# Optimization experiments

Hardware: AMD Instinct MI355X
Metric: run time of the kernel (lower is better)

The kernel has to match this reference:

```python
import jax, jax.numpy as jnp
import numpy as np

NUM_LATENTS = 8192
LATENT_DIM = 256


def setup_inputs() -> dict:
    key = jax.random.key(0)
    kx, kw = jax.random.split(key)
    x = jax.random.normal(kx, (32, 512, LATENT_DIM), dtype=jnp.float32)
    # codebook init: uniform(-1/K, 1/K), matching nn.Embedding init in the module
    bound = 1.0 / NUM_LATENTS
    codebook = jax.random.uniform(
        kw, (NUM_LATENTS, LATENT_DIM), dtype=jnp.float32, minval=-bound, maxval=bound
    )
    return {"x": x, "codebook": codebook}


def reference(x, codebook):
    # torch.cdist(x, W) followed by argmin. Since sqrt is monotone, argmin over
    # squared Euclidean distance gives identical indices; we expand
    x2 = jnp.sum(x * x, axis=-1, keepdims=True)              # [B, T, 1]
    w2 = jnp.sum(codebook * codebook, axis=-1)               # [K]
    xw = jnp.einsum("btd,kd->btk", x, codebook)              # [B, T, K]
    dist2 = x2 - 2.0 * xw + w2                               # [B, T, K]
    indices = jnp.argmin(dist2, axis=-1)                     # [B, T] int
    z = codebook[indices]                                    # [B, T, D]
    # straight-through estimator: z_q = x + stop_grad(z - x)
    z_q = x + jax.lax.stop_gradient(z - x)
    return (z_q, z, x, indices)
```

## Files before the change

### kernel.cpp

```cpp
#include <hip/hip_runtime.h>
#include <hip/hip_bf16.h>
#include <cstddef>
#include <cstdint>

#define M_TOK   16384
#define N_CODE  8192
#define K_DIM   256
#define NSPLIT  4
#define BM      128
#define BN      256
#define BK      32
#define KSTEPS  (K_DIM / BK)
#define TILES   ((N_CODE / NSPLIT) / BN)
#define TOTAL_STEPS (TILES * KSTEPS)
#define STEP_BYTES 49152
#define XH_OFF 0
#define XL_OFF 8192
#define WH_OFF 16384
#define WL_OFF 32768

typedef short bf16x8 __attribute__((ext_vector_type(8)));
typedef float f32x4  __attribute__((ext_vector_type(4)));

__device__ __forceinline__ unsigned short f2bf_rne(float f) {
    unsigned u = __float_as_uint(f);
    unsigned r = u + 0x7FFFu + ((u >> 16) & 1u);
    return (unsigned short)(r >> 16);
}
__device__ __forceinline__ float bf2f(unsigned short h) {
    union { unsigned u; float f; } c; c.u = ((unsigned)h) << 16; return c.f;
}

__device__ __forceinline__ void gload16(const void* g, void* l) {
    __builtin_amdgcn_global_load_lds(
        (const __attribute__((address_space(1))) void*)g,
        (__attribute__((address_space(3))) void*)l, 16, 0, 0);
}

__global__ void vq_prep(const float* __restrict__ x, const float* __restrict__ cb,
                        unsigned short* __restrict__ xh, unsigned short* __restrict__ xl,
                        unsigned short* __restrict__ wh, unsigned short* __restrict__ wl,
                        float* __restrict__ x2, float* __restrict__ w2) {
    int gt   = blockIdx.x * blockDim.x + threadIdx.x;
    int row  = gt >> 6;
    int lane = gt & 63;
    if (row >= M_TOK + N_CODE) return;
    const float* src; unsigned short *dh, *dl; float* dn;
    if (row < M_TOK) {
        src = x + (size_t)row * K_DIM;
        dh = xh + (size_t)row * K_DIM; dl = xl + (size_t)row * K_DIM; dn = x2 + row;
    } else {
        int r = row - M_TOK;
        src = cb + (size_t)r * K_DIM;
        dh = wh + (size_t)r * K_DIM; dl = wl + (size_t)r * K_DIM; dn = w2 + r;
    }
    float4 v = ((const float4*)src)[lane];
    unsigned short h0 = f2bf_rne(v.x), h1 = f2bf_rne(v.y);
    unsigned short h2 = f2bf_rne(v.z), h3 = f2bf_rne(v.w);
    unsigned short l0 = f2bf_rne(v.x - bf2f(h0)), l1 = f2bf_rne(v.y - bf2f(h1));
    unsigned short l2 = f2bf_rne(v.z - bf2f(h2)), l3 = f2bf_rne(v.w - bf2f(h3));
    ushort4 hv; hv.x = h0; hv.y = h1; hv.z = h2; hv.w = h3;
    ushort4 lv; lv.x = l0; lv.y = l1; lv.z = l2; lv.w = l3;
    ((ushort4*)dh)[lane] = hv;
    ((ushort4*)dl)[lane] = lv;
    float s = v.x*v.x + v.y*v.y + v.z*v.z + v.w*v.w;
    #pragma unroll
    for (int off = 32; off > 0; off >>= 1) s += __shfl_down(s, off);
    if (lane == 0) *dn = s;
}

__global__ __launch_bounds__(512, 2)
void vq_main_mfma(const unsigned short* __restrict__ xh, const unsigned short* __restrict__ xl,
                  const unsigned short* __restrict__ wh, const unsigned short* __restrict__ wl,
                  const float* __restrict__ x2, const float* __restrict__ w2,
                  float* __restrict__ pminv, int* __restrict__ pmini) {
    __shared__ __align__(1024) char sb[3][STEP_BYTES];
    __shared__ float red_d[BM][4];
    __shared__ int   red_i[BM][4];

    const int fid   = blockIdx.y * NSPLIT + blockIdx.x;
    const int xcd   = fid & 7;
    const int split = xcd & 3;
    const int mtile = ((xcd >> 2) << 6) + (fid >> 3);
    const int gm    = mtile * BM;

    const int tid   = threadIdx.x;
    const int w     = tid >> 6;
    const int lane  = tid & 63;
    const int wr    = w >> 2;
    const int wc    = w & 3;
    const int quad  = lane >> 4;
    const int l15   = lane & 15;

    const int srow4 = lane >> 2;
    const int sg    = (lane & 3) ^ ((lane >> 3) & 3);

    const char* xhp = (const char*)xh;
    const char* xlp = (const char*)xl;
    const char* whp = (const char*)wh;
    const char* wlp = (const char*)wl;

    const size_t xg0 = (size_t)(gm + w*16 + srow4) * (K_DIM*2) + (size_t)sg*16;
    const size_t wg0 = (size_t)(w*32 + srow4) * (K_DIM*2) + (size_t)sg*16;
    const size_t wg1 = wg0 + (size_t)16 * (K_DIM*2);
    const unsigned lx = (unsigned)w*1024 + (unsigned)lane*16;
    const unsigned lw = (unsigned)w*2048 + (unsigned)lane*16;

    float x2r[16];
    #pragma unroll
    for (int rt = 0; rt < 4; ++rt)
        #pragma unroll
        for (int reg = 0; reg < 4; ++reg)
            x2r[rt*4+reg] = x2[gm + wr*64 + rt*16 + quad*4 + reg];

    float minv[16];
    int   mini[16];
    #pragma unroll
    for (int i = 0; i < 16; ++i) { minv[i] = 3.4e38f; mini[i] = 0; }

    auto stage = [&](int s, char* buf) {
        const size_t kb  = (size_t)(s & (KSTEPS-1)) * (BK*2);
        const size_t nbo = ((size_t)(split*(N_CODE/NSPLIT) + (s >> 3) * BN)) * (K_DIM*2);
        gload16(xhp + xg0 + kb,        buf + XH_OFF + lx);
        gload16(xlp + xg0 + kb,        buf + XL_OFF + lx);
        gload16(whp + nbo + wg0 + kb,  buf + WH_OFF + lw);
        gload16(whp + nbo + wg1 + kb,  buf + WH_OFF + lw + 1024);
        gload16(wlp + nbo + wg0 + kb,  buf + WL_OFF + lw);
        gload16(wlp + nbo + wg1 + kb,  buf + WL_OFF + lw + 1024);
    };

    char* bufA = &sb[0][0];
    char* bufB = &sb[1][0];
    char* bufC = &sb[2][0];
    stage(0, bufA); stage(1, bufB); stage(2, bufC);

    const int slb = (quad ^ ((l15 >> 1) & 3)) * 16;

    for (int tile = 0; tile < TILES; ++tile) {
        f32x4 acc[4][4];
        #pragma unroll
        for (int rt = 0; rt < 4; ++rt)
            #pragma unroll
            for (int ct = 0; ct < 4; ++ct)
                acc[rt][ct] = (f32x4){0.f, 0.f, 0.f, 0.f};

        for (int kcs = 0; kcs < KSTEPS; ++kcs) {
            const int step = tile * KSTEPS + kcs;

            if (step < TOTAL_STEPS - 2)       asm volatile("s_waitcnt vmcnt(12)" ::: "memory");
            else if (step == TOTAL_STEPS - 2) asm volatile("s_waitcnt vmcnt(6)" ::: "memory");
            else                              asm volatile("s_waitcnt vmcnt(0)" ::: "memory");
            __builtin_amdgcn_s_barrier();
            __builtin_amdgcn_sched_barrier(0);

            bf16x8 ah[4], al[4], bh[4], bl[4];
            #pragma unroll
            for (int rt = 0; rt < 4; ++rt) {
                const int off = (wr*64 + rt*16 + l15) * (BK*2) + slb;
                ah[rt] = *(const bf16x8*)(bufA + XH_OFF + off);
                al[rt] = *(const bf16x8*)(bufA + XL_OFF + off);
            }
            #pragma unroll
            for (int ct = 0; ct < 4; ++ct) {
                const int off = (wc*64 + ct*16 + l15) * (BK*2) + slb;
                bh[ct] = *(const bf16x8*)(bufA + WH_OFF + off);
                bl[ct] = *(const bf16x8*)(bufA + WL_OFF + off);
            }
            asm volatile("s_waitcnt lgkmcnt(0)" ::: "memory");
            __builtin_amdgcn_sched_barrier(0);
            __builtin_amdgcn_s_barrier();
            __builtin_amdgcn_sched_barrier(0);

            const int sn = step + 3;
            if (sn < TOTAL_STEPS) stage(sn, bufA);

            __builtin_amdgcn_s_setprio(1);
            #pragma unroll
            for (int rt = 0; rt < 4; ++rt)
                #pragma unroll
                for (int ct = 0; ct < 4; ++ct) {
                    acc[rt][ct] = __builtin_amdgcn_mfma_f32_16x16x32_bf16(al[rt], bh[ct], acc[rt][ct], 0, 0, 0);
                    acc[rt][ct] = __builtin_amdgcn_mfma_f32_16x16x32_bf16(ah[rt], bl[ct], acc[rt][ct], 0, 0, 0);
                    acc[rt][ct] = __builtin_amdgcn_mfma_f32_16x16x32_bf16(ah[rt], bh[ct], acc[rt][ct], 0, 0, 0);
                }
            __builtin_amdgcn_s_setprio(0);

            char* t = bufA; bufA = bufB; bufB = bufC; bufC = t;
        }

        const int nb = split * (N_CODE / NSPLIT) + tile * BN;
        float w2c[4];
        int   cidx[4];
        #pragma unroll
        for (int ct = 0; ct < 4; ++ct) {
            cidx[ct] = nb + wc*64 + ct*16 + l15;
            w2c[ct]  = w2[cidx[ct]];
        }
        #pragma unroll
        for (int rt = 0; rt < 4; ++rt)
            #pragma unroll
            for (int ct = 0; ct < 4; ++ct) {
                #pragma unroll
                for (int reg = 0; reg < 4; ++reg) {
                    float d = (x2r[rt*4+reg] - 2.0f * acc[rt][ct][reg]) + w2c[ct];
                    int r16 = rt*4 + reg;
                    if (d < minv[r16]) { minv[r16] = d; mini[r16] = cidx[ct]; }
                }
            }
    }

    #pragma unroll
    for (int r16 = 0; r16 < 16; ++r16) {
        float d  = minv[r16];
        int   ix = mini[r16];
        #pragma unroll
        for (int off = 1; off < 16; off <<= 1) {
            float od = __shfl_xor(d, off);
            int   oi = __shfl_xor(ix, off);
            if (od < d || (od == d && oi < ix)) { d = od; ix = oi; }
        }
        if (l15 == 0) {
            int row_local = wr*64 + (r16 >> 2)*16 + quad*4 + (r16 & 3);
            red_d[row_local][wc] = d;
            red_i[row_local][wc] = ix;
        }
    }
    __syncthreads();
    if (tid < BM) {
        float d  = red_d[tid][0];
        int   ix = red_i[tid][0];
        #pragma unroll
        for (int j = 1; j < 4; ++j) {
            float dj = red_d[tid][j];
            int   ij = red_i[tid][j];
            if (dj < d || (dj == d && ij < ix)) { d = dj; ix = ij; }
        }
        pminv[(size_t)(gm + tid) * NSPLIT + split] = d;
        pmini[(size_t)(gm + tid) * NSPLIT + split] = ix;
    }
}

__global__ void vq_gather(const float* __restrict__ x, const float* __restrict__ cb,
                          const float* __restrict__ pminv, const int* __restrict__ pmini,
                          float* __restrict__ out) {
    int t = blockIdx.x * blockDim.x + threadIdx.x;
    int m = t >> 6;
    int q = t & 63;

    float d  = pminv[(size_t)m * NSPLIT + (q & (NSPLIT-1))];
    int   ix = pmini[(size_t)m * NSPLIT + (q & (NSPLIT-1))];
    #pragma unroll
    for (int off = 1; off < NSPLIT; off <<= 1) {
        float od = __shfl_xor(d, off);
        int   oi = __shfl_xor(ix, off);
        if (od < d || (od == d && oi < ix)) { d = od; ix = oi; }
    }

    float4 xv = ((const float4*)x)[t];
    float4 zv = ((const float4*)cb)[(size_t)ix * 64 + q];
    float4 zq;
    zq.x = xv.x + (zv.x - xv.x);
    zq.y = xv.y + (zv.y - xv.y);
    zq.z = xv.z + (zv.z - xv.z);
    zq.w = xv.w + (zv.w - xv.w);
    float4* o = (float4*)out;
    const int ELEM4 = M_TOK * 64;
    o[t]           = zq;
    o[t + ELEM4]   = zv;
    o[t + 2*ELEM4] = xv;
    if (q == 0) out[(size_t)3 * M_TOK * K_DIM + m] = (float)ix;
}

extern "C" void kernel_launch(void* const* d_in, const int* in_sizes, int n_in,
                              void* d_out, int out_size, void* d_ws, size_t ws_size,
                              hipStream_t stream) {
    const float* x  = (const float*)d_in[0];
    const float* cb = (const float*)d_in[1];
    float* out = (float*)d_out;

    char* p = (char*)d_ws;
    unsigned short* xh = (unsigned short*)p;  p += (size_t)M_TOK  * K_DIM * 2;
    unsigned short* xl = (unsigned short*)p;  p += (size_t)M_TOK  * K_DIM * 2;
    unsigned short* wh = (unsigned short*)p;  p += (size_t)N_CODE * K_DIM * 2;
    unsigned short* wl = (unsigned short*)p;  p += (size_t)N_CODE * K_DIM * 2;
    float* x2    = (float*)p;  p += (size_t)M_TOK * 4;
    float* w2    = (float*)p;  p += (size_t)N_CODE * 4;
    float* pminv = (float*)p;  p += (size_t)M_TOK * NSPLIT * 4;
    int*   pmini = (int*)p;    p += (size_t)M_TOK * NSPLIT * 4;

    {
        int waves = M_TOK + N_CODE;
        vq_prep<<<(waves * 64 + 255) / 256, 256, 0, stream>>>(x, cb, xh, xl, wh, wl, x2, w2);
    }
    {
        dim3 grid(NSPLIT, M_TOK / BM);
        vq_main_mfma<<<grid, 512, 0, stream>>>(xh, xl, wh, wl, x2, w2, pminv, pmini);
    }
    {
        int t = M_TOK * (K_DIM / 4);
        vq_gather<<<t / 256, 256, 0, stream>>>(x, cb, pminv, pmini, out);
    }
}
```

Baseline: 295.7 us.

## Register double-buffer LDS fragments and stage norms in shared memory

The main loop now loads the next k-step's A/B fragments from LDS into a second register set while MFMAs run on the current set. This drops one barrier per step and hides LDS read latency behind compute. The MFMAs are regrouped into three passes (lo*hi, hi*lo, hi*hi). The x2 and w2 norms are prefetched into shared memory with async global-to-LDS loads instead of being kept in registers or read from global per tile. In exchange it uses twice as many fragment registers, which risks spills at the 512x2 launch bounds, and the vmcnt accounting changes with the extra loads.

```diff
diff --git a/kernel.cpp b/kernel.cpp
--- a/kernel.cpp
+++ b/kernel.cpp
@@ -75,6 +75,8 @@
                   const float* __restrict__ x2, const float* __restrict__ w2,
                   float* __restrict__ pminv, int* __restrict__ pmini) {
     __shared__ __align__(1024) char sb[3][STEP_BYTES];
+    __shared__ float x2s[BM];
+    __shared__ float w2s[N_CODE/NSPLIT];
     __shared__ float red_d[BM][4];
     __shared__ int   red_i[BM][4];
 
@@ -103,111 +105,146 @@
     const size_t xg0 = (size_t)(gm + w*16 + srow4) * (K_DIM*2) + (size_t)sg*16;
     const size_t wg0 = (size_t)(w*32 + srow4) * (K_DIM*2) + (size_t)sg*16;
     const size_t wg1 = wg0 + (size_t)16 * (K_DIM*2);
-    const unsigned lx = (unsigned)w*1024 + (unsigned)lane*16;
-    const unsigned lw = (unsigned)w*2048 + (unsigned)lane*16;
-
-    float x2r[16];
-    #pragma unroll
-    for (int rt = 0; rt < 4; ++rt)
-        #pragma unroll
-        for (int reg = 0; reg < 4; ++reg)
-            x2r[rt*4+reg] = x2[gm + wr*64 + rt*16 + quad*4 + reg];
-
-    float minv[16];
-    int   mini[16];
-    #pragma unroll
-    for (int i = 0; i < 16; ++i) { minv[i] = 3.4e38f; mini[i] = 0; }
+    const unsigned lxu = (unsigned)w*1024;
+    const unsigned lwu = (unsigned)w*2048;
 
     auto stage = [&](int s, char* buf) {
         const size_t kb  = (size_t)(s & (KSTEPS-1)) * (BK*2);
         const size_t nbo = ((size_t)(split*(N_CODE/NSPLIT) + (s >> 3) * BN)) * (K_DIM*2);
-        gload16(xhp + xg0 + kb,        buf + XH_OFF + lx);
-        gload16(xlp + xg0 + kb,        buf + XL_OFF + lx);
-        gload16(whp + nbo + wg0 + kb,  buf + WH_OFF + lw);
-        gload16(whp + nbo + wg1 + kb,  buf + WH_OFF + lw + 1024);
-        gload16(wlp + nbo + wg0 + kb,  buf + WL_OFF + lw);
-        gload16(wlp + nbo + wg1 + kb,  buf + WL_OFF + lw + 1024);
+        gload16(xhp + xg0 + kb,        buf + XH_OFF + lxu);
+        gload16(xlp + xg0 + kb,        buf + XL_OFF + lxu);
+        gload16(whp + nbo + wg0 + kb,  buf + WH_OFF + lwu);
+        gload16(whp + nbo + wg1 + kb,  buf + WH_OFF + lwu + 1024);
+        gload16(wlp + nbo + wg0 + kb,  buf + WL_OFF + lwu);
+        gload16(wlp + nbo + wg1 + kb,  buf + WL_OFF + lwu + 1024);
     };
 
-    char* bufA = &sb[0][0];
-    char* bufB = &sb[1][0];
-    char* bufC = &sb[2][0];
-    stage(0, bufA); stage(1, bufB); stage(2, bufC);
+    gload16((const char*)w2 + (size_t)split*(N_CODE/NSPLIT)*4 + (size_t)w*1024 + (size_t)lane*16,
+            (char*)w2s + lxu);
+    if (w == 0 && lane < 32)
+        gload16((const char*)x2 + (size_t)gm*4 + (size_t)lane*16, (char*)x2s);
+    char* cur = &sb[0][0];
+    char* nxt = &sb[1][0];
+    char* bfar = &sb[2][0];
+    stage(0, cur); stage(1, nxt); stage(2, bfar);
+    asm volatile("s_waitcnt vmcnt(12)" ::: "memory");
+    __builtin_amdgcn_s_barrier();
+    __builtin_amdgcn_sched_barrier(0);
 
     const int slb = (quad ^ ((l15 >> 1) & 3)) * 16;
 
+    bf16x8 ah0[4], al0[4], bh0[4], bl0[4];
+    bf16x8 ah1[4], al1[4], bh1[4], bl1[4];
+
+    #pragma unroll
+    for (int rt = 0; rt < 4; ++rt) {
+        const int off = (wr*64 + rt*16 + l15)*(BK*2) + slb;
+        ah0[rt] = *(const bf16x8*)(cur + XH_OFF + off);
+        al0[rt] = *(const bf16x8*)(cur + XL_OFF + off);
+    }
+    #pragma unroll
+    for (int ct = 0; ct < 4; ++ct) {
+        const int off = (wc*64 + ct*16 + l15)*(BK*2) + slb;
+        bh0[ct] = *(const bf16x8*)(cur + WH_OFF + off);
+        bl0[ct] = *(const bf16x8*)(cur + WL_OFF + off);
+    }
+    asm volatile("s_waitcnt lgkmcnt(0)" ::: "memory");
+    __builtin_amdgcn_sched_barrier(0);
+
+    float minv[16];
+    int   mini[16];
+    #pragma unroll
+    for (int i = 0; i < 16; ++i) { minv[i] = 3.4e38f; mini[i] = 0; }
+
+    f32x4 acc[4][4];
+
+#define ITER(TILE, KCS, AHc, ALc, BHc, BLc, AHl, ALl, BHl, BLl)                       \
+    do {                                                                              \
+        const int step_ = (TILE)*KSTEPS + (KCS);                                      \
+        if (step_ < TOTAL_STEPS-2) { asm volatile("s_waitcnt vmcnt(6)" ::: "memory"); } \
+        else                       { asm volatile("s_waitcnt vmcnt(0)" ::: "memory"); } \
+        __builtin_amdgcn_s_barrier();                                                 \
+        __builtin_amdgcn_sched_barrier(0);                                            \
+        if ((TILE) != TILES-1 || (KCS) != KSTEPS-1) {                                 \
+            _Pragma("unroll")                                                         \
+            for (int rt = 0; rt < 4; ++rt) {                                          \
+                const int off_ = (wr*64 + rt*16 + l15)*(BK*2) + slb;                  \
+                AHl[rt] = *(const bf16x8*)(nxt + XH_OFF + off_);                      \
+                ALl[rt] = *(const bf16x8*)(nxt + XL_OFF + off_);                      \
+            }                                                                         \
+            _Pragma("unroll")                                                         \
+            for (int ct = 0; ct < 4; ++ct) {                                          \
+                const int off_ = (wc*64 + ct*16 + l15)*(BK*2) + slb;                  \
+                BHl[ct] = *(const bf16x8*)(nxt + WH_OFF + off_);                      \
+                BLl[ct] = *(const bf16x8*)(nxt + WL_OFF + off_);                      \
+            }                                                                         \
+        }                                                                             \
+        if (step_ <= TOTAL_STEPS-4) stage(step_+3, cur);                              \
+        __builtin_amdgcn_sched_barrier(0);                                            \
+        __builtin_amdgcn_s_setprio(1);                                                \
+        _Pragma("unroll")                                                             \
+        for (int rt = 0; rt < 4; ++rt)                                                \
+            _Pragma("unroll")                                                         \
+            for (int ct = 0; ct < 4; ++ct)                                            \
+                acc[rt][ct] = __builtin_amdgcn_mfma_f32_16x16x32_bf16(ALc[rt], BHc[ct], acc[rt][ct], 0, 0, 0); \
+        _Pragma("unroll")                                                             \
+        for (int rt = 0; rt < 4; ++rt)                                                \
+            _Pragma("unroll")                                                         \
+            for (int ct = 0; ct < 4; ++ct)                                            \
+                acc[rt][ct] = __builtin_amdgcn_mfma_f32_16x16x32_bf16(AHc[rt], BLc[ct], acc[rt][ct], 0, 0, 0); \
+        _Pragma("unroll")                                                             \
+        for (int rt = 0; rt < 4; ++rt)                                                \
+            _Pragma("unroll")                                                         \
+            for (int ct = 0; ct < 4; ++ct)                                            \
+                acc[rt][ct] = __builtin_amdgcn_mfma_f32_16x16x32_bf16(AHc[rt], BHc[ct], acc[rt][ct], 0, 0, 0); \
+        __builtin_amdgcn_s_setprio(0);                                                \
+        asm volatile("s_waitcnt lgkmcnt(0)" ::: "memory");                            \
+        __builtin_amdgcn_sched_barrier(0);                                            \
+        { char* t_ = cur; cur = nxt; nxt = bfar; bfar = t_; }                         \
+    } while (0)
+
     for (int tile = 0; tile < TILES; ++tile) {
-        f32x4 acc[4][4];
         #pragma unroll
         for (int rt = 0; rt < 4; ++rt)
             #pragma unroll
             for (int ct = 0; ct < 4; ++ct)
                 acc[rt][ct] = (f32x4){0.f, 0.f, 0.f, 0.f};
 
-        for (int kcs = 0; kcs < KSTEPS; ++kcs) {
-            const int step = tile * KSTEPS + kcs;
-
-            if (step < TOTAL_STEPS - 2)       asm volatile("s_waitcnt vmcnt(12)" ::: "memory");
-            else if (step == TOTAL_STEPS - 2) asm volatile("s_waitcnt vmcnt(6)" ::: "memory");
-            else                              asm volatile("s_waitcnt vmcnt(0)" ::: "memory");
-            __builtin_amdgcn_s_barrier();
-            __builtin_amdgcn_sched_barrier(0);
-
-            bf16x8 ah[4], al[4], bh[4], bl[4];
-            #pragma unroll
-            for (int rt = 0; rt < 4; ++rt) {
-                const int off = (wr*64 + rt*16 + l15) * (BK*2) + slb;
-                ah[rt] = *(const bf16x8*)(bufA + XH_OFF + off);
-                al[rt] = *(const bf16x8*)(bufA + XL_OFF + off);
-            }
-            #pragma unroll
-            for (int ct = 0; ct < 4; ++ct) {
-                const int off = (wc*64 + ct*16 + l15) * (BK*2) + slb;
-                bh[ct] = *(const bf16x8*)(bufA + WH_OFF + off);
-                bl[ct] = *(const bf16x8*)(bufA + WL_OFF + off);
-            }
-            asm volatile("s_waitcnt lgkmcnt(0)" ::: "memory");
-            __builtin_amdgcn_sched_barrier(0);
-            __builtin_amdgcn_s_barrier();
-            __builtin_amdgcn_sched_barrier(0);
-
-            const int sn = step + 3;
-            if (sn < TOTAL_STEPS) stage(sn, bufA);
-
-            __builtin_amdgcn_s_setprio(1);
-            #pragma unroll
-            for (int rt = 0; rt < 4; ++rt)
-                #pragma unroll
-                for (int ct = 0; ct < 4; ++ct) {
-                    acc[rt][ct] = __builtin_amdgcn_mfma_f32_16x16x32_bf16(al[rt], bh[ct], acc[rt][ct], 0, 0, 0);
-                    acc[rt][ct] = __builtin_amdgcn_mfma_f32_16x16x32_bf16(ah[rt], bl[ct], acc[rt][ct], 0, 0, 0);
-                    acc[rt][ct] = __builtin_amdgcn_mfma_f32_16x16x32_bf16(ah[rt], bh[ct], acc[rt][ct], 0, 0, 0);
-                }
-            __builtin_amdgcn_s_setprio(0);
-
-            char* t = bufA; bufA = bufB; bufB = bufC; bufC = t;
-        }
+        ITER(tile, 0, ah0, al0, bh0, bl0, ah1, al1, bh1, bl1);
+        ITER(tile, 1, ah1, al1, bh1, bl1, ah0, al0, bh0, bl0);
+        ITER(tile, 2, ah0, al0, bh0, bl0, ah1, al1, bh1, bl1);
+        ITER(tile, 3, ah1, al1, bh1, bl1, ah0, al0, bh0, bl0);
+        ITER(tile, 4, ah0, al0, bh0, bl0, ah1, al1, bh1, bl1);
+        ITER(tile, 5, ah1, al1, bh1, bl1, ah0, al0, bh0, bl0);
+        ITER(tile, 6, ah0, al0, bh0, bl0, ah1, al1, bh1, bl1);
+        ITER(tile, 7, ah1, al1, bh1, bl1, ah0, al0, bh0, bl0);
 
         const int nb = split * (N_CODE / NSPLIT) + tile * BN;
+        f32x4 x2v[4];
+        #pragma unroll
+        for (int rt = 0; rt < 4; ++rt)
+            x2v[rt] = *(const f32x4*)((const char*)x2s + (wr*64 + rt*16 + quad*4)*4);
         float w2c[4];
         int   cidx[4];
         #pragma unroll
         for (int ct = 0; ct < 4; ++ct) {
             cidx[ct] = nb + wc*64 + ct*16 + l15;
-            w2c[ct]  = w2[cidx[ct]];
+            w2c[ct]  = w2s[tile*BN + wc*64 + ct*16 + l15];
         }
+        asm volatile("s_waitcnt lgkmcnt(0)" ::: "memory");
         #pragma unroll
         for (int rt = 0; rt < 4; ++rt)
             #pragma unroll
             for (int ct = 0; ct < 4; ++ct) {
                 #pragma unroll
                 for (int reg = 0; reg < 4; ++reg) {
-                    float d = (x2r[rt*4+reg] - 2.0f * acc[rt][ct][reg]) + w2c[ct];
+                    float d = (x2v[rt][reg] - 2.0f * acc[rt][ct][reg]) + w2c[ct];
                     int r16 = rt*4 + reg;
                     if (d < minv[r16]) { minv[r16] = d; mini[r16] = cidx[ct]; }
                 }
             }
     }
+#undef ITER
 
     #pragma unroll
     for (int r16 = 0; r16 < 16; ++r16) {
```

Measured after the change: 403.3 us. +36.4%, slower.
